# Optimization experiments

Measured on AMD Instinct MI355X. Metric: run time of the kernel, lower is better.

The kernel has to match this reference:

```python
import jax, jax.numpy as jnp
import numpy as np

D_MODEL = 1024
NUM_HEADS = 16
HEAD_DIM = D_MODEL // NUM_HEADS


def setup_inputs() -> dict:
    key = jax.random.key(0)
    ks = jax.random.split(key, 9)
    s = 1.0 / np.sqrt(D_MODEL)
    inp = {
        "x": jax.random.normal(ks[0], (4, 2048, D_MODEL), dtype=jnp.float32),
        "wq": jax.random.uniform(ks[1], (D_MODEL, D_MODEL), jnp.float32, -s, s),
        "bq": jax.random.uniform(ks[2], (D_MODEL,), jnp.float32, -s, s),
        "wk": jax.random.uniform(ks[3], (D_MODEL, D_MODEL), jnp.float32, -s, s),
        "bk": jax.random.uniform(ks[4], (D_MODEL,), jnp.float32, -s, s),
        "wv": jax.random.uniform(ks[5], (D_MODEL, D_MODEL), jnp.float32, -s, s),
        "bv": jax.random.uniform(ks[6], (D_MODEL,), jnp.float32, -s, s),
        "wo": jax.random.uniform(ks[7], (D_MODEL, D_MODEL), jnp.float32, -s, s),
        "bo": jax.random.uniform(ks[8], (D_MODEL,), jnp.float32, -s, s),
    }
    return inp


def _split_heads(t):
    # [B, S, D] -> [B, H, S, Dh]
    b, s, _ = t.shape
    return t.reshape(b, s, NUM_HEADS, HEAD_DIM).transpose(0, 2, 1, 3)


def reference(x, wq, bq, wk, bk, wv, bv, wo, bo):
    b, s, _ = x.shape
    q = _split_heads(x @ wq.T + bq)
    k = _split_heads(x @ wk.T + bk)
    v = _split_heads(x @ wv.T + bv)
    scale = 1.0 / np.sqrt(HEAD_DIM).astype(np.float32)
    scores = jnp.einsum('bhqd,bhkd->bhqk', q, k) * scale  # [B,H,S,S]
    probs = jax.nn.softmax(scores, axis=-1)
    ctx = jnp.einsum('bhqk,bhkd->bhqd', probs, v)  # [B,H,S,Dh]
    ctx = ctx.transpose(0, 2, 1, 3).reshape(b, s, D_MODEL)
    return ctx @ wo.T + bo
```

## Files before the change

### kernel.cpp

```cpp
#include <hip/hip_runtime.h>
#include <stdint.h>

typedef short bf16x8 __attribute__((ext_vector_type(8)));
typedef float f32x4 __attribute__((ext_vector_type(4)));

#define D_MODEL 1024
#define NHEAD   16
#define HDIM    64
#define BATCH   4
#define SEQ     2048
#define NTOK    (BATCH * SEQ)

#define BM 128
#define BN 128
#define BK 64

#define LOG2E 1.44269504088896340736f

__device__ __forceinline__ unsigned short f2bf_fast(float f) {
  return (unsigned short)((__float_as_uint(f) + 0x8000u) >> 16);
}

__device__ __forceinline__ void gload_lds16(const unsigned short* g, unsigned short* l) {
  __builtin_amdgcn_global_load_lds((const __attribute__((address_space(1))) void*)g,
                                   (__attribute__((address_space(3))) void*)l,
                                   16, 0, 0);
}

__global__ __launch_bounds__(256) void cvt_all(
    const float* __restrict__ x, const float* __restrict__ wq,
    const float* __restrict__ wk, const float* __restrict__ wv,
    const float* __restrict__ wo, unsigned short* __restrict__ dst) {
  long i = ((long)blockIdx.x * 256 + threadIdx.x) * 4;
  const float* src; long off;
  if (i < 8388608)       { src = x;  off = 0; }
  else if (i < 9437184)  { src = wq; off = 8388608; }
  else if (i < 10485760) { src = wk; off = 9437184; }
  else if (i < 11534336) { src = wv; off = 10485760; }
  else                   { src = wo; off = 11534336; }
  const float4 v = *(const float4*)(src + (i - off));
  ushort4 o = make_ushort4(f2bf_fast(v.x), f2bf_fast(v.y), f2bf_fast(v.z), f2bf_fast(v.w));
  *(ushort4*)(dst + i) = o;
}

__device__ __forceinline__ void gemm_bt_mainloop(
    const unsigned short* __restrict__ Abase,
    const unsigned short* __restrict__ Bbase,
    int lda, int ldb, int K,
    unsigned short* sA, unsigned short* sB,
    f32x4 acc[4][4]) {
  const int tid = threadIdx.x;
  const int wave = tid >> 6, lane = tid & 63;
  const int ln15 = lane & 15, quad = lane >> 4;
  const int wy = wave >> 1, wx = wave & 1;

#pragma unroll
  for (int mt = 0; mt < 4; ++mt)
#pragma unroll
    for (int nt = 0; nt < 4; ++nt)
      acc[mt][nt] = (f32x4){0.f, 0.f, 0.f, 0.f};

  for (int k0 = 0; k0 < K; k0 += BK) {
    __syncthreads();
#pragma unroll
    for (int i = 0; i < 4; ++i) {
      int chunk = i * 256 + wave * 64 + lane;
      int row = chunk >> 3, c = (chunk & 7) ^ (row & 7);
      gload_lds16(Abase + row * lda + k0 + c * 8, sA + (i * 256 + wave * 64) * 8);
      gload_lds16(Bbase + row * ldb + k0 + c * 8, sB + (i * 256 + wave * 64) * 8);
    }
    __syncthreads();
#pragma unroll
    for (int ks = 0; ks < 2; ++ks) {
      const int swz = ((ks * 4 + quad) ^ (ln15 & 7)) * 8;
      bf16x8 af[4], bfv[4];
#pragma unroll
      for (int t = 0; t < 4; ++t)
        af[t] = *(const bf16x8*)(sA + (64 * wy + 16 * t + ln15) * BK + swz);
#pragma unroll
      for (int t = 0; t < 4; ++t)
        bfv[t] = *(const bf16x8*)(sB + (64 * wx + 16 * t + ln15) * BK + swz);
#pragma unroll
      for (int mt = 0; mt < 4; ++mt)
#pragma unroll
        for (int nt = 0; nt < 4; ++nt)
          acc[mt][nt] = __builtin_amdgcn_mfma_f32_16x16x32_bf16(af[mt], bfv[nt], acc[mt][nt], 0, 0, 0);
    }
  }
}

#define TSTR 136
__global__ __launch_bounds__(256) void qkv_gemm(
    const unsigned short* __restrict__ xb,
    const unsigned short* __restrict__ wall,
    const float* __restrict__ bq, const float* __restrict__ bk, const float* __restrict__ bv,
    unsigned short* __restrict__ Qb, unsigned short* __restrict__ Kb,
    unsigned short* __restrict__ Vt) {
  const int n0g = blockIdx.y * BN;
  const int z = n0g >> 10;
  const int n0 = n0g & 1023;
  const float* bias = (z == 0) ? bq : (z == 1) ? bk : bv;
  const int m0 = blockIdx.x * BM;

  __shared__ __align__(16) unsigned char smem[BM * TSTR * 2];
  unsigned short* sA = (unsigned short*)smem;
  unsigned short* sB = (unsigned short*)(smem + BM * BK * 2);
  unsigned short* sT = (unsigned short*)smem;

  f32x4 acc[4][4];
  gemm_bt_mainloop(xb + (size_t)m0 * D_MODEL, wall + (size_t)n0g * D_MODEL,
                   D_MODEL, D_MODEL, D_MODEL, sA, sB, acc);

  const int tid = threadIdx.x;
  const int lane = tid & 63, wave = tid >> 6;
  const int ln15 = lane & 15, quad = lane >> 4;
  const int wy = wave >> 1, wx = wave & 1;
  const int b = m0 >> 11;

  if (z == 2) {
    __syncthreads();
#pragma unroll
    for (int mt = 0; mt < 4; ++mt)
#pragma unroll
      for (int nt = 0; nt < 4; ++nt) {
        int j = 64 * wx + 16 * nt + ln15;
        float bj = bias[n0 + j];
#pragma unroll
        for (int r = 0; r < 4; r += 2) {
          int tok = 64 * wy + 16 * mt + quad * 4 + r;
          unsigned int pk = (unsigned int)f2bf_fast(acc[mt][nt][r] + bj) |
                            ((unsigned int)f2bf_fast(acc[mt][nt][r + 1] + bj) << 16);
          *(unsigned int*)(sT + j * TSTR + tok) = pk;
        }
      }
    __syncthreads();
    const int sbase = (m0 & 2047) + (tid & 15) * 8;
#pragma unroll
    for (int i = 0; i < 8; ++i) {
      int j = (tid >> 4) + i * 16;
      int feature = n0 + j;
      int h = feature >> 6, d = feature & 63;
      bf16x8 val = *(const bf16x8*)(sT + j * TSTR + (tid & 15) * 8);
      *(bf16x8*)(Vt + (((size_t)(b * NHEAD + h)) * HDIM + d) * SEQ + sbase) = val;
    }
  } else {
    const float scale = (z == 0) ? 0.125f * LOG2E : 1.0f;
    unsigned short* dst = (z == 0) ? Qb : Kb;
    __syncthreads();
    float bj[4];
#pragma unroll
    for (int nt = 0; nt < 4; ++nt) bj[nt] = bias[n0 + 64 * wx + 16 * nt + ln15];
#pragma unroll
    for (int mt = 0; mt < 4; ++mt)
#pragma unroll
      for (int nt = 0; nt < 4; ++nt)
#pragma unroll
        for (int r = 0; r < 4; ++r) {
          int tok = 64 * wy + 16 * mt + quad * 4 + r;
          int j = 64 * wx + 16 * nt + ln15;
          sT[tok * TSTR + j] = f2bf_fast((acc[mt][nt][r] + bj[nt]) * scale);
        }
    __syncthreads();
    const int srow = m0 & 2047;
#pragma unroll
    for (int i = 0; i < 8; ++i) {
      int tok = (tid >> 4) + i * 16;
      int jj = (tid & 15) * 8;
      bf16x8 val = *(const bf16x8*)(sT + tok * TSTR + jj);
      int feature = n0 + jj;
      int h = feature >> 6, d = feature & 63;
      *(bf16x8*)(dst + (((size_t)(b * NHEAD + h)) * SEQ + srow + tok) * HDIM + d) = val;
    }
  }
}

#define PSTR 72
__global__ __launch_bounds__(256, 4) void attn_kernel(
    const unsigned short* __restrict__ Qb,
    const unsigned short* __restrict__ Kb,
    const unsigned short* __restrict__ Vt,
    unsigned short* __restrict__ ctxb) {
  const int qb = blockIdx.x;
  const int bh = blockIdx.y;
  const int s0 = qb * 128;
  const int tid = threadIdx.x, wave = tid >> 6, lane = tid & 63;
  const int ln15 = lane & 15, quad = lane >> 4;

  __shared__ __align__(16) unsigned short sK[64 * 64], sV[64 * 64], sP[128 * PSTR];

  const unsigned short* Qg = Qb + (size_t)bh * SEQ * HDIM;
  const unsigned short* Kg = Kb + (size_t)bh * SEQ * HDIM;
  const unsigned short* Vg = Vt + (size_t)bh * HDIM * SEQ;

  bf16x8 qf[2][2];
#pragma unroll
  for (int mt = 0; mt < 2; ++mt)
#pragma unroll
    for (int ks = 0; ks < 2; ++ks)
      qf[mt][ks] = *(const bf16x8*)(Qg + (s0 + 32 * wave + 16 * mt + ln15) * HDIM + ks * 32 + quad * 8);

  const int chunk0 = wave * 64 + lane;
  const int row0 = chunk0 >> 3, c0 = (chunk0 & 7) ^ (row0 & 7);
  const int chunk1 = 256 + wave * 64 + lane;
  const int row1 = chunk1 >> 3, c1 = (chunk1 & 7) ^ (row1 & 7);
  const int krow0 = ((row0 & 15) << 2) | (row0 >> 4);
  const int krow1 = ((row1 & 15) << 2) | (row1 >> 4);
  const unsigned short* Kp0 = Kg + krow0 * HDIM + c0 * 8;
  const unsigned short* Kp1 = Kg + krow1 * HDIM + c1 * 8;
  const unsigned short* Vp0 = Vg + row0 * SEQ + c0 * 8;
  const unsigned short* Vp1 = Vg + row1 * SEQ + c1 * 8;
  unsigned short* dK0 = sK + chunk0 * 8;
  unsigned short* dK1 = sK + chunk1 * 8;
  unsigned short* dV0 = sV + chunk0 * 8;
  unsigned short* dV1 = sV + chunk1 * 8;

  unsigned short* sPw = sP + (32 * wave + 4 * quad) * PSTR + ln15 * 4;

  const f32x4 zero4 = (f32x4){0.f, 0.f, 0.f, 0.f};

  float l_part[8];
  f32x4 O[2][4];
#pragma unroll
  for (int i = 0; i < 8; ++i) l_part[i] = 0.f;
#pragma unroll
  for (int mt = 0; mt < 2; ++mt)
#pragma unroll
    for (int dt = 0; dt < 4; ++dt) O[mt][dt] = (f32x4){0.f, 0.f, 0.f, 0.f};

  for (int k0 = 0; k0 < SEQ; k0 += 64) {
    __syncthreads();
    gload_lds16(Kp0 + k0 * HDIM, dK0);
    gload_lds16(Kp1 + k0 * HDIM, dK1);
    gload_lds16(Vp0 + k0, dV0);
    gload_lds16(Vp1 + k0, dV1);
    __syncthreads();

    f32x4 sc[2][4];
    {
      const int swz = (quad ^ (ln15 & 7)) * 8;
#pragma unroll
      for (int nt = 0; nt < 4; ++nt) {
        bf16x8 bk8 = *(const bf16x8*)(sK + (16 * nt + ln15) * 64 + swz);
#pragma unroll
        for (int mt = 0; mt < 2; ++mt)
          sc[mt][nt] = __builtin_amdgcn_mfma_f32_16x16x32_bf16(qf[mt][0], bk8, zero4, 0, 0, 0);
      }
    }
    {
      const int swz = ((4 + quad) ^ (ln15 & 7)) * 8;
#pragma unroll
      for (int nt = 0; nt < 4; ++nt) {
        bf16x8 bk8 = *(const bf16x8*)(sK + (16 * nt + ln15) * 64 + swz);
#pragma unroll
        for (int mt = 0; mt < 2; ++mt)
          sc[mt][nt] = __builtin_amdgcn_mfma_f32_16x16x32_bf16(qf[mt][1], bk8, sc[mt][nt], 0, 0, 0);
      }
    }

#pragma unroll
    for (int mt = 0; mt < 2; ++mt)
#pragma unroll
      for (int r = 0; r < 4; ++r) {
        float p0 = __builtin_amdgcn_exp2f(sc[mt][0][r]);
        float p1 = __builtin_amdgcn_exp2f(sc[mt][1][r]);
        float p2 = __builtin_amdgcn_exp2f(sc[mt][2][r]);
        float p3 = __builtin_amdgcn_exp2f(sc[mt][3][r]);
        l_part[mt * 4 + r] += (p0 + p1) + (p2 + p3);
        unsigned int a0 = __float_as_uint(p0) + 0x8000u;
        unsigned int a1 = __float_as_uint(p1) + 0x8000u;
        unsigned int a2 = __float_as_uint(p2) + 0x8000u;
        unsigned int a3 = __float_as_uint(p3) + 0x8000u;
        uint2 pk;
        pk.x = __builtin_amdgcn_perm(a1, a0, 0x07060302u);
        pk.y = __builtin_amdgcn_perm(a3, a2, 0x07060302u);
        *(uint2*)(sPw + (16 * mt + r) * PSTR) = pk;
      }

#pragma unroll
    for (int ks = 0; ks < 2; ++ks) {
      const int swz = ((ks * 4 + quad) ^ (ln15 & 7)) * 8;
      bf16x8 ap[2];
#pragma unroll
      for (int mt = 0; mt < 2; ++mt)
        ap[mt] = *(const bf16x8*)(sP + (32 * wave + 16 * mt + ln15) * PSTR + ks * 32 + quad * 8);
#pragma unroll
      for (int dt = 0; dt < 4; ++dt) {
        bf16x8 bv8 = *(const bf16x8*)(sV + (16 * dt + ln15) * 64 + swz);
#pragma unroll
        for (int mt = 0; mt < 2; ++mt)
          O[mt][dt] = __builtin_amdgcn_mfma_f32_16x16x32_bf16(ap[mt], bv8, O[mt][dt], 0, 0, 0);
      }
    }
  }

  const int b = bh >> 4, h = bh & 15;
#pragma unroll
  for (int mt = 0; mt < 2; ++mt)
#pragma unroll
    for (int r = 0; r < 4; ++r) {
      float l = l_part[mt * 4 + r];
      l += __shfl_xor(l, 1);
      l += __shfl_xor(l, 2);
      l += __shfl_xor(l, 4);
      l += __shfl_xor(l, 8);
      float inv = 1.0f / l;
      int token = b * SEQ + s0 + 32 * wave + 16 * mt + quad * 4 + r;
#pragma unroll
      for (int dt = 0; dt < 4; ++dt)
        ctxb[(size_t)token * D_MODEL + h * HDIM + 16 * dt + ln15] = f2bf_fast(O[mt][dt][r] * inv);
    }
}

__global__ __launch_bounds__(256) void oproj_kernel(
    const unsigned short* __restrict__ ctxb,
    const unsigned short* __restrict__ wob,
    const float* __restrict__ bo,
    float* __restrict__ out) {
  const int m0 = blockIdx.x * BM, n0 = blockIdx.y * BN;
  __shared__ __align__(16) unsigned short sA[BM * BK], sB[BN * BK];
  f32x4 acc[4][4];
  gemm_bt_mainloop(ctxb + (size_t)m0 * D_MODEL, wob + (size_t)n0 * D_MODEL,
                   D_MODEL, D_MODEL, D_MODEL, sA, sB, acc);

  const int lane = threadIdx.x & 63, wave = threadIdx.x >> 6;
  const int ln15 = lane & 15, quad = lane >> 4;
  const int wy = wave >> 1, wx = wave & 1;
#pragma unroll
  for (int mt = 0; mt < 4; ++mt)
#pragma unroll
    for (int nt = 0; nt < 4; ++nt)
#pragma unroll
      for (int r = 0; r < 4; ++r) {
        int n = m0 + 64 * wy + 16 * mt + quad * 4 + r;
        int j = n0 + 64 * wx + 16 * nt + ln15;
        out[(size_t)n * D_MODEL + j] = acc[mt][nt][r] + bo[j];
      }
}

extern "C" void kernel_launch(void* const* d_in, const int* in_sizes, int n_in,
                              void* d_out, int out_size, void* d_ws, size_t ws_size,
                              hipStream_t stream) {
  const float* x  = (const float*)d_in[0];
  const float* wq = (const float*)d_in[1];
  const float* bq = (const float*)d_in[2];
  const float* wk = (const float*)d_in[3];
  const float* bk = (const float*)d_in[4];
  const float* wv = (const float*)d_in[5];
  const float* bv = (const float*)d_in[6];
  const float* wo = (const float*)d_in[7];
  const float* bo = (const float*)d_in[8];
  float* out = (float*)d_out;

  unsigned short* ws   = (unsigned short*)d_ws;
  unsigned short* xb   = ws;
  unsigned short* wall = ws + 8388608;
  unsigned short* wob  = ws + 11534336;
  unsigned short* Qb   = ws + 12582912;
  unsigned short* Kb   = ws + 20971520;
  unsigned short* Vtb  = ws + 29360128;
  unsigned short* ctxb = ws + 37748736;

  cvt_all<<<12288, 256, 0, stream>>>(x, wq, wk, wv, wo, ws);

  qkv_gemm<<<dim3(64, 24), 256, 0, stream>>>(xb, wall, bq, bk, bv, Qb, Kb, Vtb);
  attn_kernel<<<dim3(16, 64), 256, 0, stream>>>(Qb, Kb, Vtb, ctxb);
  oproj_kernel<<<dim3(64, 8), 256, 0, stream>>>(ctxb, wob, bo, out);
}
```

Measured before the change: 270.4 us.

## Overlap K/V tile loads with attention compute and remap block order

Restructures the attention loop so the next K tile is fetched right after the QK^T MFMAs and the next V tile right after the PV MFMAs. Each fetch is waited on with partial vmcnt counts and raw s_barrier, replacing the two full __syncthreads around each load. Adds s_setprio around the MFMA sections and remaps the flat block index so consecutive blocks spread across batch-heads, aiming for better L2/XCD locality. This relies on the barriers and vmcnt counts being exactly right, and single buffering still forces the next load to wait for the current tile's consumers.

```diff
diff --git a/kernel.cpp b/kernel.cpp
--- a/kernel.cpp
+++ b/kernel.cpp
@@ -180,8 +180,10 @@
     const unsigned short* __restrict__ Kb,
     const unsigned short* __restrict__ Vt,
     unsigned short* __restrict__ ctxb) {
-  const int qb = blockIdx.x;
-  const int bh = blockIdx.y;
+  const int flat = blockIdx.y * gridDim.x + blockIdx.x;
+  const int sbid = (flat & 7) * 128 + (flat >> 3);
+  const int qb = sbid & 15;
+  const int bh = sbid >> 4;
   const int s0 = qb * 128;
   const int tid = threadIdx.x, wave = tid >> 6, lane = tid & 63;
   const int ln15 = lane & 15, quad = lane >> 4;
@@ -227,34 +229,46 @@
 #pragma unroll
     for (int dt = 0; dt < 4; ++dt) O[mt][dt] = (f32x4){0.f, 0.f, 0.f, 0.f};
 
+  gload_lds16(Kp0, dK0);
+  gload_lds16(Kp1, dK1);
+  gload_lds16(Vp0, dV0);
+  gload_lds16(Vp1, dV1);
+
   for (int k0 = 0; k0 < SEQ; k0 += 64) {
-    __syncthreads();
-    gload_lds16(Kp0 + k0 * HDIM, dK0);
-    gload_lds16(Kp1 + k0 * HDIM, dK1);
-    gload_lds16(Vp0 + k0, dV0);
-    gload_lds16(Vp1 + k0, dV1);
-    __syncthreads();
+    const int kn = k0 + 64;
+
+    asm volatile("s_waitcnt vmcnt(2)" ::: "memory");
+    __builtin_amdgcn_s_barrier();
 
     f32x4 sc[2][4];
+    __builtin_amdgcn_s_setprio(1);
     {
-      const int swz = (quad ^ (ln15 & 7)) * 8;
+      const int swk = (quad ^ (ln15 & 7)) * 8;
 #pragma unroll
       for (int nt = 0; nt < 4; ++nt) {
-        bf16x8 bk8 = *(const bf16x8*)(sK + (16 * nt + ln15) * 64 + swz);
+        bf16x8 bk8 = *(const bf16x8*)(sK + (16 * nt + ln15) * 64 + swk);
 #pragma unroll
         for (int mt = 0; mt < 2; ++mt)
           sc[mt][nt] = __builtin_amdgcn_mfma_f32_16x16x32_bf16(qf[mt][0], bk8, zero4, 0, 0, 0);
       }
     }
     {
-      const int swz = ((4 + quad) ^ (ln15 & 7)) * 8;
+      const int swk = ((4 + quad) ^ (ln15 & 7)) * 8;
 #pragma unroll
       for (int nt = 0; nt < 4; ++nt) {
-        bf16x8 bk8 = *(const bf16x8*)(sK + (16 * nt + ln15) * 64 + swz);
+        bf16x8 bk8 = *(const bf16x8*)(sK + (16 * nt + ln15) * 64 + swk);
 #pragma unroll
         for (int mt = 0; mt < 2; ++mt)
           sc[mt][nt] = __builtin_amdgcn_mfma_f32_16x16x32_bf16(qf[mt][1], bk8, sc[mt][nt], 0, 0, 0);
       }
+    }
+    __builtin_amdgcn_s_setprio(0);
+
+    __builtin_amdgcn_sched_barrier(0);
+    __builtin_amdgcn_s_barrier();
+    if (kn < SEQ) {
+      gload_lds16(Kp0 + kn * HDIM, dK0);
+      gload_lds16(Kp1 + kn * HDIM, dK1);
     }
 
 #pragma unroll
@@ -276,20 +290,33 @@
         *(uint2*)(sPw + (16 * mt + r) * PSTR) = pk;
       }
 
+    if (kn < SEQ) asm volatile("s_waitcnt vmcnt(2)" ::: "memory");
+    else          asm volatile("s_waitcnt vmcnt(0)" ::: "memory");
+    __builtin_amdgcn_s_barrier();
+
+    __builtin_amdgcn_s_setprio(1);
 #pragma unroll
     for (int ks = 0; ks < 2; ++ks) {
-      const int swz = ((ks * 4 + quad) ^ (ln15 & 7)) * 8;
+      const int swv = ((ks * 4 + quad) ^ (ln15 & 7)) * 8;
       bf16x8 ap[2];
 #pragma unroll
       for (int mt = 0; mt < 2; ++mt)
         ap[mt] = *(const bf16x8*)(sP + (32 * wave + 16 * mt + ln15) * PSTR + ks * 32 + quad * 8);
 #pragma unroll
       for (int dt = 0; dt < 4; ++dt) {
-        bf16x8 bv8 = *(const bf16x8*)(sV + (16 * dt + ln15) * 64 + swz);
+        bf16x8 bv8 = *(const bf16x8*)(sV + (16 * dt + ln15) * 64 + swv);
 #pragma unroll
         for (int mt = 0; mt < 2; ++mt)
           O[mt][dt] = __builtin_amdgcn_mfma_f32_16x16x32_bf16(ap[mt], bv8, O[mt][dt], 0, 0, 0);
       }
+    }
+    __builtin_amdgcn_s_setprio(0);
+
+    __builtin_amdgcn_sched_barrier(0);
+    __builtin_amdgcn_s_barrier();
+    if (kn < SEQ) {
+      gload_lds16(Vp0 + kn, dV0);
+      gload_lds16(Vp1 + kn, dV1);
     }
   }
 
```

New measurement: 271.5 us. Within noise of the previous version (+0.4%).
